# Performance work log

Hardware: AMD Instinct MI355X
Metric: run time of the kernel (lower is better)

Reference implementation:

```python
import jax, jax.numpy as jnp
import numpy as np

IN_FEATURES = 1024
OUT_FEATURES = 256
BATCH = 131072
EPS = 1e-4


def setup_inputs() -> dict:
    key = jax.random.key(0)
    kx, kw, kb = jax.random.split(key, 3)
    x = jax.random.normal(kx, (BATCH, IN_FEATURES), dtype=jnp.float32)
    # nn.Linear default init: U(-1/sqrt(in), 1/sqrt(in)) for both W and b
    bound = 1.0 / np.sqrt(IN_FEATURES)
    W = jax.random.uniform(kw, (OUT_FEATURES, IN_FEATURES), dtype=jnp.float32, minval=-bound, maxval=bound)
    b = jax.random.uniform(kb, (OUT_FEATURES,), dtype=jnp.float32, minval=-bound, maxval=bound)
    return {"x": x, "W": W, "b": b}


def reference(x, W, b):
    # L2-normalize each row (dim=1), matching x / (||x||_2 + 1e-4)
    norm = jnp.sqrt(jnp.sum(x * x, axis=1, keepdims=True))
    x_dir = x / (norm + EPS)
    # Linear: x_dir @ W^T + b, then ReLU
    h = jnp.einsum('bi,oi->bo', x_dir, W) + b
    return jax.nn.relu(h)
```

## Files before the change

### kernel.cpp

```cpp
#include <hip/hip_runtime.h>


#define IN_F   1024
#define OUT_F  256
#define BATCH  131072
#define BM     128
#define NKT    16
#define EPSV   1e-4f

typedef __attribute__((ext_vector_type(8))) __bf16 bf16x8;
typedef __attribute__((ext_vector_type(4))) __bf16 bf16x4;
typedef __attribute__((ext_vector_type(4))) float  f32x4;

__device__ __forceinline__ void gload_lds16(const void* g, void* lds) {
  __builtin_amdgcn_global_load_lds(
      (const __attribute__((address_space(1))) void*)g,
      (__attribute__((address_space(3))) void*)lds, 16, 0, 0);
}

#define VM_WAIT(N) do { asm volatile("s_waitcnt vmcnt(" #N ")" ::: "memory"); \
                        __builtin_amdgcn_sched_barrier(0); } while (0)

__global__ void wconv_kernel(const float* __restrict__ W, __bf16* __restrict__ Wb) {
  const int t = blockIdx.x * blockDim.x + threadIdx.x;
  const float4 v = reinterpret_cast<const float4*>(W)[t];
  bf16x4 h;
  h[0] = (__bf16)v.x; h[1] = (__bf16)v.y; h[2] = (__bf16)v.z; h[3] = (__bf16)v.w;
  reinterpret_cast<bf16x4*>(Wb)[t] = h;
}

__global__ __launch_bounds__(1024, 4)
void ffl_kernel(const float* __restrict__ x, const __bf16* __restrict__ Wb,
                const float* __restrict__ bias, float* __restrict__ out) {
  __shared__ __align__(16) char smem[163840];
  char* const Ab[3] = {smem, smem + 32768, smem + 65536};
  char* const Bb[2] = {smem + 98304, smem + 131072};

  const int tid  = threadIdx.x;
  const int lane = tid & 63;
  const int wave = tid >> 6;
  const int wr   = wave >> 2;
  const int wc   = wave & 3;
  const int rm   = lane & 15;
  const int q    = lane >> 4;
  const size_t block_row = (size_t)blockIdx.x * BM;
  const int phg = blockIdx.x & 15;

  const float* aSrc[2]; int aDst[2];
  #pragma unroll
  for (int i = 0; i < 2; ++i) {
    const int c   = 2 * wave + i;
    const int row = 4 * c + (lane >> 4);
    const int s   = (lane & 15) ^ (row & 7);
    aSrc[i] = x + (block_row + row) * IN_F + s * 4;
    aDst[i] = c * 1024;
  }
  const int brow = 16 * wave + (lane >> 2);
  const int bs   = (lane & 3) ^ ((brow >> 1) & 3);
  const __bf16* bSrc = Wb + (size_t)brow * IN_F + bs * 8;
  const int bDst = wave * 1024;

  f32x4 acc[2][4];
  #pragma unroll
  for (int m = 0; m < 2; ++m)
    #pragma unroll
    for (int n = 0; n < 4; ++n)
      acc[m][n] = (f32x4){0.f, 0.f, 0.f, 0.f};

  float ssq0 = 0.f, ssq1 = 0.f;

  auto stageA = [&](int s) {
    const int pg = (s + phg) & 15;
    gload_lds16(aSrc[0] + pg * 64, Ab[s % 3] + aDst[0]);
    gload_lds16(aSrc[1] + pg * 64, Ab[s % 3] + aDst[1]);
  };
  auto stageB = [&](int s) {
    const int pg = (s + phg) & 15;
    gload_lds16(bSrc + pg * 64,      Bb[s & 1] + bDst);
    gload_lds16(bSrc + pg * 64 + 32, Bb[s & 1] + 16384 + bDst);
  };

  stageA(0);
  stageB(0);
  stageA(1);
  stageB(1);
  VM_WAIT(4);
  __builtin_amdgcn_s_barrier();

  #pragma unroll
  for (int kt = 0; kt < NKT; ++kt) {
    if (kt >= 1 && kt + 1 < NKT) stageB(kt + 1);
    if (kt + 2 < NKT) stageA(kt + 2);

    const char* abuf = Ab[kt % 3];
    const char* bbuf = Bb[kt & 1];

    #pragma unroll
    for (int kk = 0; kk < 2; ++kk) {
      bf16x8 aF[2];
      #pragma unroll
      for (int m = 0; m < 2; ++m) {
        const int ra = wr * 32 + m * 16 + rm;
        const char* ab = abuf + ra * 256;
        const int sw = ra & 7;
        const int g0 = kk * 8 + 2 * q;
        const f32x4 lo = *reinterpret_cast<const f32x4*>(ab + ((g0)     ^ sw) * 16);
        const f32x4 hi = *reinterpret_cast<const f32x4*>(ab + ((g0 + 1) ^ sw) * 16);
        float& ssq = m ? ssq1 : ssq0;
        ssq += lo[0]*lo[0] + lo[1]*lo[1] + lo[2]*lo[2] + lo[3]*lo[3]
             + hi[0]*hi[0] + hi[1]*hi[1] + hi[2]*hi[2] + hi[3]*hi[3];
        bf16x8 a;
        a[0]=(__bf16)lo[0]; a[1]=(__bf16)lo[1]; a[2]=(__bf16)lo[2]; a[3]=(__bf16)lo[3];
        a[4]=(__bf16)hi[0]; a[5]=(__bf16)hi[1]; a[6]=(__bf16)hi[2]; a[7]=(__bf16)hi[3];
        aF[m] = a;
      }
      const char* bhalf = bbuf + kk * 16384;
      #pragma unroll
      for (int n = 0; n < 4; ++n) {
        const int rb = wc * 64 + n * 16 + rm;
        const bf16x8 bF = *reinterpret_cast<const bf16x8*>(
            bhalf + rb * 64 + (q ^ ((rb >> 1) & 3)) * 16);
        acc[0][n] = __builtin_amdgcn_mfma_f32_16x16x32_bf16(aF[0], bF, acc[0][n], 0, 0, 0);
        acc[1][n] = __builtin_amdgcn_mfma_f32_16x16x32_bf16(aF[1], bF, acc[1][n], 0, 0, 0);
      }
    }

    if (kt < 14) { VM_WAIT(2); } else { VM_WAIT(0); }
    __builtin_amdgcn_s_barrier();
  }

  ssq0 += __shfl_xor(ssq0, 16); ssq0 += __shfl_xor(ssq0, 32);
  ssq1 += __shfl_xor(ssq1, 16); ssq1 += __shfl_xor(ssq1, 32);
  float* norms = reinterpret_cast<float*>(smem + 163328);
  if (wc == 0 && q == 0) {
    norms[wr * 32 + rm]      = 1.0f / (sqrtf(ssq0) + EPSV);
    norms[wr * 32 + 16 + rm] = 1.0f / (sqrtf(ssq1) + EPSV);
  }
  __syncthreads();

  float* stg = reinterpret_cast<float*>(smem);
  const int col0 = wc * 64 + rm;
  #pragma unroll
  for (int n = 0; n < 4; ++n) {
    const float bn = bias[col0 + n * 16];
    #pragma unroll
    for (int m = 0; m < 2; ++m) {
      #pragma unroll
      for (int j = 0; j < 4; ++j) {
        const int lr = wr * 32 + m * 16 + q * 4 + j;
        stg[lr * 260 + col0 + n * 16] = fmaxf(acc[m][n][j] * norms[lr] + bn, 0.f);
      }
    }
  }
  __syncthreads();

  const int r = tid >> 3, p = tid & 7;
  const float* srow = stg + r * 260;
  float* orow = out + (block_row + r) * OUT_F;
  #pragma unroll
  for (int i = 0; i < 8; ++i) {
    const int f = i * 8 + p;
    const f32x4 v = *reinterpret_cast<const f32x4*>(srow + f * 4);
    *reinterpret_cast<f32x4*>(orow + f * 4) = v;
  }
}

extern "C" void kernel_launch(void* const* d_in, const int* in_sizes, int n_in,
                              void* d_out, int out_size, void* d_ws, size_t ws_size,
                              hipStream_t stream) {
  const float* x = (const float*)d_in[0];
  const float* W = (const float*)d_in[1];
  const float* b = (const float*)d_in[2];
  float* out = (float*)d_out;
  __bf16* Wb = (__bf16*)d_ws;

  wconv_kernel<<<(OUT_F * IN_F / 4) / 256, 256, 0, stream>>>(W, Wb);
  ffl_kernel<<<BATCH / BM, 1024, 0, stream>>>(x, Wb, b, out);
}
```

Before: 172.6 us.

## Halve block tile to 64 rows, 512 threads, with staggered large-chunk A staging

Shrinks the batch tile to 64 rows per block with 512 threads, and replaces per-step 64-column A loads with 256-column chunks whose row loads are spread across the following k-steps in a two-buffer pipeline. B staging is now one 32-wide k-slice per step, double-buffered. The intent is more blocks in flight and fewer barrier-bound stages relative to the x stream, at the cost of more k iterations, more barriers, and reloading W once per 64 rows instead of once per 128 rows.

Result: slower. 222.2 us (+28.8%).

```diff
diff --git a/kernel.cpp b/kernel.cpp
--- a/kernel.cpp
+++ b/kernel.cpp
@@ -4,8 +4,8 @@
 #define IN_F   1024
 #define OUT_F  256
 #define BATCH  131072
-#define BM     128
-#define NKT    16
+#define BM     64
+#define NKT    32
 #define EPSV   1e-4f
 
 typedef __attribute__((ext_vector_type(8))) __bf16 bf16x8;
@@ -29,12 +29,12 @@
   reinterpret_cast<bf16x4*>(Wb)[t] = h;
 }
 
-__global__ __launch_bounds__(1024, 4)
+__global__ __launch_bounds__(512, 2)
 void ffl_kernel(const float* __restrict__ x, const __bf16* __restrict__ Wb,
                 const float* __restrict__ bias, float* __restrict__ out) {
   __shared__ __align__(16) char smem[163840];
-  char* const Ab[3] = {smem, smem + 32768, smem + 65536};
-  char* const Bb[2] = {smem + 98304, smem + 131072};
+  char* const Ab[2] = {smem, smem + 65536};
+  char* const Bb[2] = {smem + 131072, smem + 147456};
 
   const int tid  = threadIdx.x;
   const int lane = tid & 63;
@@ -44,21 +44,17 @@
   const int rm   = lane & 15;
   const int q    = lane >> 4;
   const size_t block_row = (size_t)blockIdx.x * BM;
-  const int phg = blockIdx.x & 15;
+  const int phg = blockIdx.x & 3;
 
-  const float* aSrc[2]; int aDst[2];
+  const __bf16* bSrc[2]; int bDst[2];
   #pragma unroll
   for (int i = 0; i < 2; ++i) {
-    const int c   = 2 * wave + i;
-    const int row = 4 * c + (lane >> 4);
-    const int s   = (lane & 15) ^ (row & 7);
-    aSrc[i] = x + (block_row + row) * IN_F + s * 4;
-    aDst[i] = c * 1024;
+    const int c    = 2 * wave + i;
+    const int brow = 16 * c + (lane >> 2);
+    const int bs   = (lane & 3) ^ ((brow >> 1) & 3);
+    bSrc[i] = Wb + (size_t)brow * IN_F + bs * 8;
+    bDst[i] = c * 1024;
   }
-  const int brow = 16 * wave + (lane >> 2);
-  const int bs   = (lane & 3) ^ ((brow >> 1) & 3);
-  const __bf16* bSrc = Wb + (size_t)brow * IN_F + bs * 8;
-  const int bDst = wave * 1024;
 
   f32x4 acc[2][4];
   #pragma unroll
@@ -69,69 +65,75 @@
 
   float ssq0 = 0.f, ssq1 = 0.f;
 
-  auto stageA = [&](int s) {
-    const int pg = (s + phg) & 15;
-    gload_lds16(aSrc[0] + pg * 64, Ab[s % 3] + aDst[0]);
-    gload_lds16(aSrc[1] + pg * 64, Ab[s % 3] + aDst[1]);
+  auto stageAinst = [&](int g, int i) {
+    const int pg   = (g + phg) & 3;
+    const int rloc = 8 * wave + i;
+    gload_lds16(x + (block_row + rloc) * IN_F + pg * 256 + ((lane ^ i) << 2),
+                Ab[g & 1] + rloc * 1024);
   };
   auto stageB = [&](int s) {
-    const int pg = (s + phg) & 15;
-    gload_lds16(bSrc + pg * 64,      Bb[s & 1] + bDst);
-    gload_lds16(bSrc + pg * 64 + 32, Bb[s & 1] + 16384 + bDst);
+    const int pk = ((((s >> 3) + phg) & 3) << 3) + (s & 7);
+    gload_lds16(bSrc[0] + pk * 32, Bb[s & 1] + bDst[0]);
+    gload_lds16(bSrc[1] + pk * 32, Bb[s & 1] + bDst[1]);
   };
 
-  stageA(0);
+  #pragma unroll
+  for (int i = 0; i < 8; ++i) stageAinst(0, i);
   stageB(0);
-  stageA(1);
-  stageB(1);
-  VM_WAIT(4);
+  VM_WAIT(0);
   __builtin_amdgcn_s_barrier();
 
   #pragma unroll
   for (int kt = 0; kt < NKT; ++kt) {
-    if (kt >= 1 && kt + 1 < NKT) stageB(kt + 1);
-    if (kt + 2 < NKT) stageA(kt + 2);
+    const int r  = kt & 7;
+    const int gn = (kt >> 3) + 1;
 
-    const char* abuf = Ab[kt % 3];
+    if (kt + 1 < NKT) stageB(kt + 1);
+    if (gn < 4) {
+      if (r == 0) { stageAinst(gn, 0); stageAinst(gn, 1); stageAinst(gn, 2); }
+      else if (r <= 5) { stageAinst(gn, r + 2); }
+    }
+
+    const char* abuf = Ab[(kt >> 3) & 1];
     const char* bbuf = Bb[kt & 1];
+    const int   w8   = (kt & 7) * 8;
+
+    bf16x8 aF[2];
+    #pragma unroll
+    for (int m = 0; m < 2; ++m) {
+      const int ra = wr * 32 + m * 16 + rm;
+      const char* ab = abuf + ra * 1024;
+      const int sw = ra & 7;
+      const int g0 = w8 + 2 * q;
+      const f32x4 lo = *reinterpret_cast<const f32x4*>(ab + ((g0)     ^ sw) * 16);
+      const f32x4 hi = *reinterpret_cast<const f32x4*>(ab + ((g0 + 1) ^ sw) * 16);
+      float& ssq = m ? ssq1 : ssq0;
+      ssq += lo[0]*lo[0] + lo[1]*lo[1] + lo[2]*lo[2] + lo[3]*lo[3]
+           + hi[0]*hi[0] + hi[1]*hi[1] + hi[2]*hi[2] + hi[3]*hi[3];
+      bf16x8 a;
+      a[0]=(__bf16)lo[0]; a[1]=(__bf16)lo[1]; a[2]=(__bf16)lo[2]; a[3]=(__bf16)lo[3];
+      a[4]=(__bf16)hi[0]; a[5]=(__bf16)hi[1]; a[6]=(__bf16)hi[2]; a[7]=(__bf16)hi[3];
+      aF[m] = a;
+    }
 
     #pragma unroll
-    for (int kk = 0; kk < 2; ++kk) {
-      bf16x8 aF[2];
-      #pragma unroll
-      for (int m = 0; m < 2; ++m) {
-        const int ra = wr * 32 + m * 16 + rm;
-        const char* ab = abuf + ra * 256;
-        const int sw = ra & 7;
-        const int g0 = kk * 8 + 2 * q;
-        const f32x4 lo = *reinterpret_cast<const f32x4*>(ab + ((g0)     ^ sw) * 16);
-        const f32x4 hi = *reinterpret_cast<const f32x4*>(ab + ((g0 + 1) ^ sw) * 16);
-        float& ssq = m ? ssq1 : ssq0;
-        ssq += lo[0]*lo[0] + lo[1]*lo[1] + lo[2]*lo[2] + lo[3]*lo[3]
-             + hi[0]*hi[0] + hi[1]*hi[1] + hi[2]*hi[2] + hi[3]*hi[3];
-        bf16x8 a;
-        a[0]=(__bf16)lo[0]; a[1]=(__bf16)lo[1]; a[2]=(__bf16)lo[2]; a[3]=(__bf16)lo[3];
-        a[4]=(__bf16)hi[0]; a[5]=(__bf16)hi[1]; a[6]=(__bf16)hi[2]; a[7]=(__bf16)hi[3];
-        aF[m] = a;
-      }
-      const char* bhalf = bbuf + kk * 16384;
-      #pragma unroll
-      for (int n = 0; n < 4; ++n) {
-        const int rb = wc * 64 + n * 16 + rm;
-        const bf16x8 bF = *reinterpret_cast<const bf16x8*>(
-            bhalf + rb * 64 + (q ^ ((rb >> 1) & 3)) * 16);
-        acc[0][n] = __builtin_amdgcn_mfma_f32_16x16x32_bf16(aF[0], bF, acc[0][n], 0, 0, 0);
-        acc[1][n] = __builtin_amdgcn_mfma_f32_16x16x32_bf16(aF[1], bF, acc[1][n], 0, 0, 0);
-      }
+    for (int n = 0; n < 4; ++n) {
+      const int rb = wc * 64 + n * 16 + rm;
+      const bf16x8 bF = *reinterpret_cast<const bf16x8*>(
+          bbuf + rb * 64 + (q ^ ((rb >> 1) & 3)) * 16);
+      acc[0][n] = __builtin_amdgcn_mfma_f32_16x16x32_bf16(aF[0], bF, acc[0][n], 0, 0, 0);
+      acc[1][n] = __builtin_amdgcn_mfma_f32_16x16x32_bf16(aF[1], bF, acc[1][n], 0, 0, 0);
     }
 
-    if (kt < 14) { VM_WAIT(2); } else { VM_WAIT(0); }
+    if (gn < 4 && r == 0)            { VM_WAIT(3); }
+    else if (gn < 4 && r >= 1 && r <= 5) { VM_WAIT(1); }
+    else                             { VM_WAIT(0); }
     __builtin_amdgcn_s_barrier();
   }
 
   ssq0 += __shfl_xor(ssq0, 16); ssq0 += __shfl_xor(ssq0, 32);
   ssq1 += __shfl_xor(ssq1, 16); ssq1 += __shfl_xor(ssq1, 32);
-  float* norms = reinterpret_cast<float*>(smem + 163328);
+  float* norms = reinterpret_cast<float*>(smem + 131072);
   if (wc == 0 && q == 0) {
     norms[wr * 32 + rm]      = 1.0f / (sqrtf(ssq0) + EPSV);
     norms[wr * 32 + 16 + rm] = 1.0f / (sqrtf(ssq1) + EPSV);
@@ -154,9 +156,9 @@
   }
   __syncthreads();
 
-  const int r = tid >> 3, p = tid & 7;
-  const float* srow = stg + r * 260;
-  float* orow = out + (block_row + r) * OUT_F;
+  const int rr = tid >> 3, p = tid & 7;
+  const float* srow = stg + rr * 260;
+  float* orow = out + (block_row + rr) * OUT_F;
   #pragma unroll
   for (int i = 0; i < 8; ++i) {
     const int f = i * 8 + p;
@@ -175,5 +177,5 @@
   __bf16* Wb = (__bf16*)d_ws;
 
   wconv_kernel<<<(OUT_F * IN_F / 4) / 256, 256, 0, stream>>>(W, Wb);
-  ffl_kernel<<<BATCH / BM, 1024, 0, stream>>>(x, Wb, b, out);
+  ffl_kernel<<<BATCH / BM, 512, 0, stream>>>(x, Wb, b, out);
 }
```
